# Performance work log

Hardware: AMD Instinct MI355X
Metric: run time of the kernel (lower is better)

The kernel has to match this reference:

```python
import jax, jax.numpy as jnp
import numpy as np

EPS = 1e-7
ROUTING_ITERS = 3

def squash(s, axis=-1):
    # v = (|s|^2 / (1+|s|^2)) * s / |s|
    sq = jnp.sum(jnp.square(s), axis=axis, keepdims=True)
    return (sq / (1.0 + sq)) * s / jnp.sqrt(sq + EPS)

def setup_inputs() -> dict:
    key = jax.random.key(0)
    k1, k2 = jax.random.split(key)
    B, NI, DI = 64, 2048, 8      # batch, input capsules, input capsule dim
    NC, DC = 32, 16              # output capsules, output capsule dim
    x = jax.random.normal(k1, (B, NI, DI), dtype=jnp.float32)
    W = jax.random.normal(k2, (NC, NI, DC, DI), dtype=jnp.float32) * 0.05
    return {"x": x, "W": W}

def reference(x, W):
    # x: [B, NI, DI], W: [NC, NI, DC, DI]
    # tf.einsum('iabc,abdc->iabd') == project each input capsule per output capsule
    u = jnp.einsum('bif,cidf->bcid', x, W)          # [B, NC, NI, DC]
    B, NC, NI, DC = u.shape
    b = jnp.zeros((B, NC, NI, 1), dtype=u.dtype)
    v = None
    for _ in range(ROUTING_ITERS):
        c = jax.nn.softmax(b, axis=1)                # coupling over output capsules
        s = jnp.sum(c * u, axis=2, keepdims=True)    # [B, NC, 1, DC]
        v = squash(s, axis=-1)                       # [B, NC, 1, DC]
        # original: reduce_sum(matmul(u, tile(v)^T), axis=3) == NI * <u_i, v>
        agree = jnp.sum(u * v, axis=-1, keepdims=True)  # [B, NC, NI, 1]
        b = b + NI * agree
    return jnp.squeeze(v, axis=2)                    # [B, NC, DC]
```

## Files before the change

### kernel.cpp

```cpp
#include <hip/hip_runtime.h>

#define NI 2048
#define NB 64
#define NC 32
#define DC 16
#define DI 8

static constexpr float SQ_EPS = 1e-7f;

typedef float f8 __attribute__((ext_vector_type(8)));

template <int MODE>
__global__
__attribute__((amdgpu_flat_work_group_size(256, 256), amdgpu_waves_per_eu(2, 2)))
void route_pass(
    const float* __restrict__ x, const float* __restrict__ W,
    const float* __restrict__ veff, float* __restrict__ partial)
{
    __shared__ float4 wbuf[2112];
    __shared__ float4 xbuf[64];

    const int tid   = threadIdx.x;
    const int wave  = tid >> 6;
    const int lane  = tid & 63;
    const int c     = lane & 31;
    const int dg    = lane >> 5;
    const int brel0 = wave * 4;
    const int b0    = blockIdx.y * 16 + brel0;

    f8 s0 = {}, s1 = {}, s2 = {}, s3 = {};

    f8 va = {}, vb = {}, vc = {}, vd = {};
    if (MODE == 1) {
        va = *reinterpret_cast<const f8*>(veff + (((size_t)(b0+0)*2 + dg)*32 + c)*8);
        vb = *reinterpret_cast<const f8*>(veff + (((size_t)(b0+1)*2 + dg)*32 + c)*8);
        vc = *reinterpret_cast<const f8*>(veff + (((size_t)(b0+2)*2 + dg)*32 + c)*8);
        vd = *reinterpret_cast<const f8*>(veff + (((size_t)(b0+3)*2 + dg)*32 + c)*8);
    }

    for (int rnd = 0; rnd < 8; ++rnd) {
        const int i0 = blockIdx.x * 16 + rnd * 2;
        __syncthreads();
        {
            const int k   = tid & 31;
            const int p0  = tid >> 5;
            const int k10 = k & 15, kdg = k >> 4;
#pragma unroll
            for (int r = 0; r < 8; ++r) {
                const int row = r * 8 + p0;
                const int cc  = row >> 1;
                const int sub = row & 1;
                wbuf[((sub * 16 + k10) * 2 + kdg) * 33 + cc] =
                    reinterpret_cast<const float4*>(W)[
                        ((size_t)cc * NI + i0 + sub) * 32 + k];
            }
        }
        if (tid < 64) {
            const int brel = tid >> 2;
            const int q    = tid & 3;
            xbuf[tid] = reinterpret_cast<const float4*>(x)[
                ((size_t)(blockIdx.y * 16 + brel) * NI + i0) * 2 + q];
        }
        __syncthreads();

#pragma unroll
        for (int il = 0; il < 2; ++il) {
            const float4 xa0 = xbuf[(brel0+0)*4 + il*2], xa1 = xbuf[(brel0+0)*4 + il*2+1];
            const float4 xb0 = xbuf[(brel0+1)*4 + il*2], xb1 = xbuf[(brel0+1)*4 + il*2+1];
            const float4 xc0 = xbuf[(brel0+2)*4 + il*2], xc1 = xbuf[(brel0+2)*4 + il*2+1];
            const float4 xd0 = xbuf[(brel0+3)*4 + il*2], xd1 = xbuf[(brel0+3)*4 + il*2+1];

            f8 u0 = {}, u1 = {}, u2 = {}, u3 = {};
#pragma unroll
            for (int dd = 0; dd < 8; ++dd) {
                const float4 wl = wbuf[((il*16 + dd*2    )*2 + dg)*33 + c];
                const float4 wh = wbuf[((il*16 + dd*2 + 1)*2 + dg)*33 + c];
                u0[dd] = wl.x*xa0.x + wl.y*xa0.y + wl.z*xa0.z + wl.w*xa0.w
                       + wh.x*xa1.x + wh.y*xa1.y + wh.z*xa1.z + wh.w*xa1.w;
                u1[dd] = wl.x*xb0.x + wl.y*xb0.y + wl.z*xb0.z + wl.w*xb0.w
                       + wh.x*xb1.x + wh.y*xb1.y + wh.z*xb1.z + wh.w*xb1.w;
                u2[dd] = wl.x*xc0.x + wl.y*xc0.y + wl.z*xc0.z + wl.w*xc0.w
                       + wh.x*xc1.x + wh.y*xc1.y + wh.z*xc1.z + wh.w*xc1.w;
                u3[dd] = wl.x*xd0.x + wl.y*xd0.y + wl.z*xd0.z + wl.w*xd0.w
                       + wh.x*xd1.x + wh.y*xd1.y + wh.z*xd1.z + wh.w*xd1.w;
            }

            if (MODE == 0) {
                const float cu = 1.0f / 32.0f;
                s0 += u0 * cu; s1 += u1 * cu; s2 += u2 * cu; s3 += u3 * cu;
            } else {
#pragma unroll
                for (int pr = 0; pr < 2; ++pr) {
                    const f8& ue = pr ? u2 : u0;
                    const f8& uo = pr ? u3 : u1;
                    const f8& ve = pr ? vc : va;
                    const f8& vo = pr ? vd : vb;
                    float pe = 0.0f, po = 0.0f;
#pragma unroll
                    for (int k = 0; k < 8; ++k) {
                        pe += ue[k] * ve[k];
                        po += uo[k] * vo[k];
                    }
                    const float send = (dg == 0) ? po : pe;
                    const float recv = __shfl_xor(send, 32);
                    float a = ((dg == 0) ? pe : po) + recv;
                    float m = a;
#pragma unroll
                    for (int off = 16; off >= 1; off >>= 1)
                        m = fmaxf(m, __shfl_xor(m, off));
                    const float e = __expf(a - m);
                    float t = e;
#pragma unroll
                    for (int off = 16; off >= 1; off >>= 1)
                        t += __shfl_xor(t, off);
                    const float mine  = e / t;
                    const float other = __shfl_xor(mine, 32);
                    const float ce = (dg == 0) ? mine : other;
                    const float co = (dg == 0) ? other : mine;
                    if (pr == 0) { s0 += u0 * ce; s1 += u1 * co; }
                    else         { s2 += u2 * ce; s3 += u3 * co; }
                }
            }
        }
    }

    {
        const int pblk = blockIdx.y * gridDim.x + blockIdx.x;
        float* gp = partial +
            (((size_t)pblk * 16 + brel0) * 128 + dg * 64 + c * 2) * 4;
        *reinterpret_cast<f8*>(gp)        = s0;
        *reinterpret_cast<f8*>(gp +  512) = s1;
        *reinterpret_cast<f8*>(gp + 1024) = s2;
        *reinterpret_cast<f8*>(gp + 1536) = s3;
    }
}

__global__ __launch_bounds__(512) void reduce_squash(
    const float* __restrict__ partial, float* __restrict__ veff,
    float* __restrict__ out, int phase)
{
    __shared__ float4 red[512];
    const int b   = blockIdx.x;
    const int sub = threadIdx.x & 127;
    const int ibq = threadIdx.x >> 7;
    const int c   = (sub >> 2) & 31;
    const int dq  = sub & 3;

    const float* base = partial
        + ((size_t)(b >> 4) * 2048 + (b & 15)) * 512
        + (dq >> 1) * 256 + c * 8 + (dq & 1) * 4
        + (size_t)ibq * 32 * 8192;
    float4 acc = make_float4(0.f, 0.f, 0.f, 0.f);
#pragma unroll 8
    for (int ib = 0; ib < 32; ++ib) {
        const float4 p = *reinterpret_cast<const float4*>(base + (size_t)ib * 8192);
        acc.x += p.x; acc.y += p.y; acc.z += p.z; acc.w += p.w;
    }
    red[threadIdx.x] = acc;
    __syncthreads();
    if (threadIdx.x < 128) {
        const float4 a1 = red[sub + 128];
        const float4 a2 = red[sub + 256];
        const float4 a3 = red[sub + 384];
        acc.x += a1.x + a2.x + a3.x;
        acc.y += a1.y + a2.y + a3.y;
        acc.z += a1.z + a2.z + a3.z;
        acc.w += a1.w + a2.w + a3.w;

        float sq = acc.x*acc.x + acc.y*acc.y + acc.z*acc.z + acc.w*acc.w;
        sq += __shfl_xor(sq, 1);
        sq += __shfl_xor(sq, 2);
        const float scale = sq / ((1.0f + sq) * sqrtf(sq + SQ_EPS));

        if (phase == 3) {
            float4* op = reinterpret_cast<float4*>(out + ((size_t)b * NC + c) * DC + dq * 4);
            *op = make_float4(scale*acc.x, scale*acc.y, scale*acc.z, scale*acc.w);
        } else {
            const float ns = scale * (float)NI;
            float4* vp = reinterpret_cast<float4*>(
                veff + (((size_t)b * 2 + (dq >> 1)) * 32 + c) * 8 + (dq & 1) * 4);
            if (phase == 1) {
                *vp = make_float4(ns*acc.x, ns*acc.y, ns*acc.z, ns*acc.w);
            } else {
                float4 old = *vp;
                *vp = make_float4(old.x + ns*acc.x, old.y + ns*acc.y,
                                  old.z + ns*acc.z, old.w + ns*acc.w);
            }
        }
    }
}

extern "C" void kernel_launch(void* const* d_in, const int* in_sizes, int n_in,
                              void* d_out, int out_size, void* d_ws, size_t ws_size,
                              hipStream_t stream) {
    (void)in_sizes; (void)n_in; (void)out_size; (void)ws_size;
    const float* x = (const float*)d_in[0];
    const float* W = (const float*)d_in[1];

    float* partial = (float*)d_ws;
    float* veff    = (float*)d_out;

    const dim3 grid(128, 4);

    route_pass<0><<<grid, 256, 0, stream>>>(x, W, nullptr, partial);
    reduce_squash<<<64, 512, 0, stream>>>(partial, veff, nullptr, 1);

    route_pass<1><<<grid, 256, 0, stream>>>(x, W, veff, partial);
    reduce_squash<<<64, 512, 0, stream>>>(partial, veff, nullptr, 2);

    route_pass<1><<<grid, 256, 0, stream>>>(x, W, veff, partial);
    reduce_squash<<<64, 512, 0, stream>>>(partial, nullptr, (float*)d_out, 3);
}
```

Measured before the change: 181.5 us.

## Double-buffer W tiles in LDS with register prefetch, preload all x

Restructures the routing pass so the next round's W slice is loaded from global memory into registers while the current round is computed from LDS, then written into a second LDS buffer. This replaces two barriers per round with one. All x values for the block's 16 input capsules are loaded up front instead of per round. The waves-per-EU hint is relaxed from a fixed 2 to a range of 1 to 8. The cost is doubled LDS for W, eight more float4 registers per thread and a larger x buffer, which may lower occupancy or cause register spills.

```diff
diff --git a/kernel.cpp b/kernel.cpp
--- a/kernel.cpp
+++ b/kernel.cpp
@@ -12,13 +12,13 @@
 
 template <int MODE>
 __global__
-__attribute__((amdgpu_flat_work_group_size(256, 256), amdgpu_waves_per_eu(2, 2)))
+__attribute__((amdgpu_flat_work_group_size(256, 256), amdgpu_waves_per_eu(1, 8)))
 void route_pass(
     const float* __restrict__ x, const float* __restrict__ W,
     const float* __restrict__ veff, float* __restrict__ partial)
 {
-    __shared__ float4 wbuf[2112];
-    __shared__ float4 xbuf[64];
+    __shared__ float4 wbuf[2][2112];
+    __shared__ float4 xbuf[512];
 
     const int tid   = threadIdx.x;
     const int wave  = tid >> 6;
@@ -27,6 +27,12 @@
     const int dg    = lane >> 5;
     const int brel0 = wave * 4;
     const int b0    = blockIdx.y * 16 + brel0;
+    const int i0    = blockIdx.x * 16;
+
+    const int k   = tid & 31;
+    const int p0  = tid >> 5;
+    const int k10 = k & 15, kdg = k >> 4;
+    const float4* Wf4 = reinterpret_cast<const float4*>(W);
 
     f8 s0 = {}, s1 = {}, s2 = {}, s3 = {};
 
@@ -38,43 +44,52 @@
         vd = *reinterpret_cast<const f8*>(veff + (((size_t)(b0+3)*2 + dg)*32 + c)*8);
     }
 
+    float4 g[8];
+
+#define STAGE_LOAD(ir0)                                                  \
+    _Pragma("unroll")                                                    \
+    for (int rr = 0; rr < 8; ++rr) {                                     \
+        const int row = rr * 8 + p0;              \
+        g[rr] = Wf4[((size_t)(row >> 1) * NI + (ir0) + (row & 1)) * 32 + k]; \
+    }
+
+#define STAGE_WRITE(buf)                                                 \
+    _Pragma("unroll")                                                    \
+    for (int rr = 0; rr < 8; ++rr) {                                     \
+        const int row = rr * 8 + p0;                                     \
+        (buf)[(((row & 1) * 16 + k10) * 2 + kdg) * 33 + (row >> 1)] = g[rr]; \
+    }
+
+    STAGE_LOAD(i0);
+    {
+        const int t0 = tid, t1 = tid + 256;
+        xbuf[t0] = reinterpret_cast<const float4*>(x)[
+            ((size_t)(blockIdx.y * 16 + (t0 >> 5)) * NI + i0 + ((t0 & 31) >> 1)) * 2 + (t0 & 1)];
+        xbuf[t1] = reinterpret_cast<const float4*>(x)[
+            ((size_t)(blockIdx.y * 16 + (t1 >> 5)) * NI + i0 + ((t1 & 31) >> 1)) * 2 + (t1 & 1)];
+    }
+    STAGE_WRITE(wbuf[0]);
+    __syncthreads();
+
+    int cur = 0;
     for (int rnd = 0; rnd < 8; ++rnd) {
-        const int i0 = blockIdx.x * 16 + rnd * 2;
-        __syncthreads();
-        {
-            const int k   = tid & 31;
-            const int p0  = tid >> 5;
-            const int k10 = k & 15, kdg = k >> 4;
-#pragma unroll
-            for (int r = 0; r < 8; ++r) {
-                const int row = r * 8 + p0;
-                const int cc  = row >> 1;
-                const int sub = row & 1;
-                wbuf[((sub * 16 + k10) * 2 + kdg) * 33 + cc] =
-                    reinterpret_cast<const float4*>(W)[
-                        ((size_t)cc * NI + i0 + sub) * 32 + k];
-            }
-        }
-        if (tid < 64) {
-            const int brel = tid >> 2;
-            const int q    = tid & 3;
-            xbuf[tid] = reinterpret_cast<const float4*>(x)[
-                ((size_t)(blockIdx.y * 16 + brel) * NI + i0) * 2 + q];
-        }
-        __syncthreads();
+        if (rnd < 7) { STAGE_LOAD(i0 + (rnd + 1) * 2); }
+
+        const float4* wb = wbuf[cur];
 
 #pragma unroll
         for (int il = 0; il < 2; ++il) {
-            const float4 xa0 = xbuf[(brel0+0)*4 + il*2], xa1 = xbuf[(brel0+0)*4 + il*2+1];
-            const float4 xb0 = xbuf[(brel0+1)*4 + il*2], xb1 = xbuf[(brel0+1)*4 + il*2+1];
-            const float4 xc0 = xbuf[(brel0+2)*4 + il*2], xc1 = xbuf[(brel0+2)*4 + il*2+1];
-            const float4 xd0 = xbuf[(brel0+3)*4 + il*2], xd1 = xbuf[(brel0+3)*4 + il*2+1];
+            const int iloc = rnd * 2 + il;
+            const float4 xa0 = xbuf[(brel0+0)*32 + iloc*2], xa1 = xbuf[(brel0+0)*32 + iloc*2+1];
+            const float4 xb0 = xbuf[(brel0+1)*32 + iloc*2], xb1 = xbuf[(brel0+1)*32 + iloc*2+1];
+            const float4 xc0 = xbuf[(brel0+2)*32 + iloc*2], xc1 = xbuf[(brel0+2)*32 + iloc*2+1];
+            const float4 xd0 = xbuf[(brel0+3)*32 + iloc*2], xd1 = xbuf[(brel0+3)*32 + iloc*2+1];
 
             f8 u0 = {}, u1 = {}, u2 = {}, u3 = {};
 #pragma unroll
             for (int dd = 0; dd < 8; ++dd) {
-                const float4 wl = wbuf[((il*16 + dd*2    )*2 + dg)*33 + c];
-                const float4 wh = wbuf[((il*16 + dd*2 + 1)*2 + dg)*33 + c];
+                const float4 wl = wb[((il*16 + dd*2    )*2 + dg)*33 + c];
+                const float4 wh = wb[((il*16 + dd*2 + 1)*2 + dg)*33 + c];
                 u0[dd] = wl.x*xa0.x + wl.y*xa0.y + wl.z*xa0.z + wl.w*xa0.w
                        + wh.x*xa1.x + wh.y*xa1.y + wh.z*xa1.z + wh.w*xa1.w;
                 u1[dd] = wl.x*xb0.x + wl.y*xb0.y + wl.z*xb0.z + wl.w*xb0.w
@@ -97,9 +112,9 @@
                     const f8& vo = pr ? vd : vb;
                     float pe = 0.0f, po = 0.0f;
 #pragma unroll
-                    for (int k = 0; k < 8; ++k) {
-                        pe += ue[k] * ve[k];
-                        po += uo[k] * vo[k];
+                    for (int kk = 0; kk < 8; ++kk) {
+                        pe += ue[kk] * ve[kk];
+                        po += uo[kk] * vo[kk];
                     }
                     const float send = (dg == 0) ? po : pe;
                     const float recv = __shfl_xor(send, 32);
@@ -122,7 +137,13 @@
                 }
             }
         }
-    }
+
+        if (rnd < 7) { STAGE_WRITE(wbuf[cur ^ 1]); }
+        __syncthreads();
+        cur ^= 1;
+    }
+#undef STAGE_LOAD
+#undef STAGE_WRITE
 
     {
         const int pblk = blockIdx.y * gridDim.x + blockIdx.x;
```

Measured after the change: 255.6 us. 1.41x slower.
